# Optimization experiments

Hardware: AMD Instinct MI355X
Metric: run time of the kernel (lower is better)

The kernel has to match this reference:

```python
import jax, jax.numpy as jnp
import numpy as np

K = 1024      # codebook_size
D = 64        # embedding_dim
DECAY = 0.99
EPS = 1e-05


def setup_inputs() -> dict:
    key = jax.random.key(0)
    k1, k2, k3 = jax.random.split(key, 3)
    z_e = jax.random.normal(k1, (16, D, 64, 64), dtype=jnp.float32)
    emb = jax.random.normal(k2, (D, K), dtype=jnp.float32) * 0.05
    emb_ema = emb  # buffer initialized as clone of emb
    counts_ema = jnp.zeros((K,), dtype=jnp.float32)
    return {"z_e": z_e, "emb": emb, "emb_ema": emb_ema, "counts_ema": counts_ema}


def reference(z_e, emb, emb_ema, counts_ema):
    B, Dd, H, W = z_e.shape
    # [B,D,H,W] -> [B*H*W, D]
    z = jnp.transpose(z_e, (0, 2, 3, 1)).reshape(-1, Dd)
    # squared L2 distance to each code: [N, K]
    dist = (z * z).sum(1, keepdims=True) - 2.0 * (z @ emb) + (emb * emb).sum(0, keepdims=True)
    idx = jnp.argmin(dist, axis=1)                      # [N]
    embeddings = emb.T[idx]                             # [N, D]
    z_q = z + jax.lax.stop_gradient(embeddings - z)     # straight-through

    # EMA codebook update (no_grad in original)
    zg = jax.lax.stop_gradient(z)
    counts = jnp.zeros((K,), dtype=emb.dtype).at[idx].add(1.0)          # one-hot column sums
    counts_ema_new = counts_ema + (1.0 - DECAY) * (counts - counts_ema)
    emb_update = jax.ops.segment_sum(zg, idx, num_segments=K).T          # [D, K]
    emb_ema_new = emb_ema + (1.0 - DECAY) * (emb_update - emb_ema)
    n = counts_ema_new.sum()
    counts_norm = (counts_ema_new + EPS) / (n + K * EPS) * n
    emb_new = emb_ema_new / counts_norm[None, :]

    z_q_out = jnp.transpose(z_q.reshape(B, H, W, Dd), (0, 3, 1, 2))      # back to [B,D,H,W]
    idx_out = idx.reshape(B, H, W)
    return z_q_out, idx_out, emb_new, emb_ema_new, counts_ema_new
```

## Files before the change

### kernel.cpp

```cpp
#include <hip/hip_runtime.h>
#include <math.h>

#define KCODES 1024
#define DDIM   64

constexpr size_t O_ZQ  = 0;
constexpr size_t O_IDX = 4194304;
constexpr size_t O_EMB = O_IDX + 65536;
constexpr size_t O_EMA = O_EMB + 65536;
constexpr size_t O_CEN = O_EMA + 65536;

constexpr size_t W_UPD   = 0;
constexpr size_t W_CNT   = 65536;
constexpr size_t W_ENORM = W_CNT + 1024;
constexpr size_t W_EMBT  = W_ENORM + 1024;
constexpr size_t W_E16   = W_EMBT + 65536;
constexpr size_t W_E16L  = W_E16 + 32768;
constexpr size_t W_FLAGN = W_E16L + 32768;
constexpr size_t W_FLAGL = W_FLAGN + 16;
constexpr int    FLAGCAP = 16384;

typedef _Float16 f16;
typedef f16 f16x8 __attribute__((ext_vector_type(8)));
typedef float f32x4 __attribute__((ext_vector_type(4)));

__global__ __launch_bounds__(256) void vq_prep(const float* __restrict__ emb,
                                               float* __restrict__ ws) {
  __shared__ float t_lds[64 * 65];
  const int tid = threadIdx.x;
  const int g   = blockIdx.x;
  const int k0  = g * 64;

  #pragma unroll
  for (int it = 0; it < 16; ++it) {
    const int idx = tid + it * 256;
    const int d   = idx >> 6;
    const int kq  = idx & 63;
    t_lds[d * 65 + kq] = emb[d * KCODES + k0 + kq];
  }
  __syncthreads();

  f16* e16h = (f16*)(ws + W_E16);
  f16* e16l = (f16*)(ws + W_E16L);
  #pragma unroll
  for (int it = 0; it < 16; ++it) {
    const int idx = tid + it * 256;
    const int k   = idx >> 6;
    const int d   = idx & 63;
    const float v = t_lds[d * 65 + k];
    ws[W_EMBT + (size_t)(k0 + k) * 64 + d] = v;
    const f16 hi = (f16)v;
    e16h[(size_t)(k0 + k) * 64 + d] = hi;
    e16l[(size_t)(k0 + k) * 64 + d] = (f16)(v - (float)hi);
  }

  if (tid < 64) {
    const int k = tid;
    float s = 0.f;
    #pragma unroll
    for (int d = 0; d < DDIM; ++d) {
      const float v = t_lds[d * 65 + k];
      s = fmaf(v, v, s);
    }
    ws[W_ENORM + k0 + k] = s;
  }

  float4* u4 = (float4*)(ws + W_UPD);
  #pragma unroll
  for (int j = 0; j < 4; ++j) u4[g * 1024 + tid + j * 256] = float4{0.f, 0.f, 0.f, 0.f};
  if (tid < 64) ws[W_CNT + k0 + tid] = 0.f;
  if (g == 0 && tid == 0) ((int*)(ws + W_FLAGN))[0] = 0;
}

#define ZP 68
__global__ __launch_bounds__(256, 4) void vq_main(
    const float* __restrict__ z_e,
    const float* __restrict__ e16hf,
    const float* __restrict__ e16lf,
    const float* __restrict__ embT,
    const float* __restrict__ eN,
    float* __restrict__ upd,
    float* __restrict__ cnt,
    int*   __restrict__ flagn,
    int*   __restrict__ flagl,
    float* __restrict__ out) {
  __shared__ float z_lds[DDIM * ZP];
  __shared__ __align__(16) f16 e_lds[128 * 64];
  __shared__ __align__(16) f16 el_lds[128 * 64];
  __shared__ __align__(16) float en_lds[128];
  __shared__ int   bidx[64];
  __shared__ float sred[33];

  const int tid  = threadIdx.x;
  const int bid  = blockIdx.x;
  const int wv   = tid >> 6;
  const int lane = tid & 63;
  const int m    = lane & 15;
  const int q    = lane >> 4;
  const int rloc = wv * 16 + m;

  const int n0  = bid * 64;
  const int b   = n0 >> 12;
  const int hw0 = n0 & 4095;
  const size_t zbase = (size_t)b * 262144 + (size_t)hw0;

  {
    const float4* z4 = (const float4*)(z_e + zbase);
    #pragma unroll
    for (int it = 0; it < 4; ++it) {
      const int f  = tid + it * 256;
      const int d  = f >> 4;
      const int r4 = f & 15;
      const float4 v = z4[(size_t)d * 1024 + r4];
      *(float4*)(z_lds + d * ZP + r4 * 4) = v;
    }
  }
  __syncthreads();

  f16x8 bf0h, bf1h, bf0l, bf1l;
  float zz = 0.f;
  #pragma unroll
  for (int j = 0; j < 8; ++j) {
    const float v0 = z_lds[(q * 8 + j) * ZP + rloc];
    const float v1 = z_lds[(32 + q * 8 + j) * ZP + rloc];
    zz = fmaf(v0, v0, zz);
    zz = fmaf(v1, v1, zz);
    const f16 h0 = (f16)v0;
    const f16 h1 = (f16)v1;
    bf0h[j] = h0;
    bf1h[j] = h1;
    bf0l[j] = (f16)(v0 - (float)h0);
    bf1l[j] = (f16)(v1 - (float)h1);
  }
  zz += __shfl_xor(zz, 16, 64);
  zz += __shfl_xor(zz, 32, 64);

  const int lcl7  = m & 7;
  const int aoff0 = m * 128 + ((q)     ^ lcl7) * 16;
  const int aoff1 = m * 128 + ((4 + q) ^ lcl7) * 16;

  float m1 = INFINITY, m2 = INFINITY;
  int   i1 = 0;
  float emax = 0.f;

  const float4* e16g4h = (const float4*)e16hf;
  const float4* e16g4l = (const float4*)e16lf;
  const float4* eNg4   = (const float4*)eN;

  #pragma unroll 1
  for (int c = 0; c < 8; ++c) {
    __syncthreads();
    #pragma unroll
    for (int i = 0; i < 4; ++i) {
      const int u  = i * 256 + tid;
      const int cl = u >> 3;
      const int db = u & 7;
      const int so = cl * 128 + ((db ^ (cl & 7)) * 16);
      const float4 vh = e16g4h[c * 1024 + u];
      const float4 vl = e16g4l[c * 1024 + u];
      *(float4*)((char*)e_lds  + so) = vh;
      *(float4*)((char*)el_lds + so) = vl;
    }
    if (tid < 32) {
      const float4 v = eNg4[c * 32 + tid];
      ((float4*)en_lds)[tid] = v;
      emax = fmaxf(emax, fmaxf(fmaxf(v.x, v.y), fmaxf(v.z, v.w)));
    }
    __syncthreads();

    #pragma unroll
    for (int t = 0; t < 8; ++t) {
      const f16x8 a0h = *(const f16x8*)((const char*)e_lds  + t * 2048 + aoff0);
      const f16x8 a1h = *(const f16x8*)((const char*)e_lds  + t * 2048 + aoff1);
      const f16x8 a0l = *(const f16x8*)((const char*)el_lds + t * 2048 + aoff0);
      const f16x8 a1l = *(const f16x8*)((const char*)el_lds + t * 2048 + aoff1);
      f32x4 acc = {0.f, 0.f, 0.f, 0.f};
      acc = __builtin_amdgcn_mfma_f32_16x16x32_f16(a0l, bf0h, acc, 0, 0, 0);
      acc = __builtin_amdgcn_mfma_f32_16x16x32_f16(a1l, bf1h, acc, 0, 0, 0);
      acc = __builtin_amdgcn_mfma_f32_16x16x32_f16(a0h, bf0l, acc, 0, 0, 0);
      acc = __builtin_amdgcn_mfma_f32_16x16x32_f16(a1h, bf1l, acc, 0, 0, 0);
      acc = __builtin_amdgcn_mfma_f32_16x16x32_f16(a0h, bf0h, acc, 0, 0, 0);
      acc = __builtin_amdgcn_mfma_f32_16x16x32_f16(a1h, bf1h, acc, 0, 0, 0);
      const float4 en4 = *(const float4*)(en_lds + t * 16 + q * 4);
      const float env[4] = {en4.x, en4.y, en4.z, en4.w};
      const int ib = c * 128 + t * 16 + q * 4;
      #pragma unroll
      for (int r = 0; r < 4; ++r) {
        const float v  = fmaf(-2.f, acc[r], env[r]);
        const bool lt  = v < m1;
        m2 = fminf(m2, fmaxf(v, m1));
        if (lt) i1 = ib + r;
        m1 = fminf(m1, v);
      }
    }
  }

  __syncthreads();
  if (tid < 32) sred[tid] = emax;
  __syncthreads();
  if (tid == 0) {
    float mx = sred[0];
    #pragma unroll
    for (int i2 = 1; i2 < 32; ++i2) mx = fmaxf(mx, sred[i2]);
    sred[32] = mx;
  }
  __syncthreads();
  const float emax2 = sred[32];

  #pragma unroll
  for (int off = 16; off <= 32; off <<= 1) {
    const float m1o = __shfl_xor(m1, off, 64);
    const float m2o = __shfl_xor(m2, off, 64);
    const int   i1o = __shfl_xor(i1, off, 64);
    const float nm2 = fminf(fminf(m2, m2o), fmaxf(m1, m1o));
    if (m1o < m1) i1 = i1o;
    m1 = fminf(m1, m1o);
    m2 = nm2;
  }

  if (lane < 16) {
    const int row = rloc;
    const float M = 1.0e-4f * sqrtf(zz) * sqrtf(emax2);
    if (m2 - m1 > M) {
      bidx[row] = i1;
      out[O_IDX + n0 + row] = (float)i1;
      atomicAdd(cnt + i1, 1.0f);
    } else {
      bidx[row] = -1;
      const int s = atomicAdd(flagn, 1);
      if (s < FLAGCAP) flagl[s] = n0 + row;
    }
  }
  __syncthreads();

  {
    const int row  = tid & 63;
    const int dgrp = tid >> 6;
    const int code = bidx[row];
    if (code >= 0) {
      const float4* er4 = (const float4*)(embT + (size_t)code * 64);
      #pragma unroll
      for (int qq = 0; qq < 4; ++qq) {
        const float4 e4 = er4[dgrp * 4 + qq];
        const float ev[4] = {e4.x, e4.y, e4.z, e4.w};
        #pragma unroll
        for (int x = 0; x < 4; ++x) {
          const int d = dgrp * 16 + qq * 4 + x;
          const float zv = z_lds[d * ZP + row];
          out[O_ZQ + zbase + (size_t)d * 4096 + row] = zv + (ev[x] - zv);
        }
      }
    }
  }

  {
    #pragma unroll 4
    for (int rr = 0; rr < 16; ++rr) {
      const int row  = wv * 16 + rr;
      const int code = bidx[row];
      if (code >= 0)
        atomicAdd(upd + (size_t)code * 64 + lane, z_lds[lane * ZP + row]);
    }
  }
}

__global__ __launch_bounds__(256) void vq_rescore(
    const float* __restrict__ z_e,
    const float* __restrict__ embT,
    const float* __restrict__ eN,
    const int* __restrict__ flagn,
    const int* __restrict__ flagl,
    float* __restrict__ upd,
    float* __restrict__ cnt,
    float* __restrict__ out) {
  __shared__ float zrow[64];
  __shared__ float wv_v[4];
  __shared__ int   wv_i[4];
  __shared__ int   bestc;

  const int tid = threadIdx.x;
  int nf = *flagn;
  if (nf > FLAGCAP) nf = FLAGCAP;

  for (int j = blockIdx.x; j < nf; j += gridDim.x) {
    __syncthreads();
    const int rowid = flagl[j];
    const int bb = rowid >> 12;
    const int hw = rowid & 4095;
    const size_t base = (size_t)bb * 262144 + (size_t)hw;
    if (tid < 64) zrow[tid] = z_e[base + (size_t)tid * 4096];
    __syncthreads();

    float bm = INFINITY;
    int   bi = 0;
    #pragma unroll
    for (int cc = 0; cc < 4; ++cc) {
      const int k = tid * 4 + cc;
      const float4* e4p = (const float4*)(embT + (size_t)k * 64);
      float a0 = 0.f, a1 = 0.f, a2 = 0.f, a3 = 0.f;
      #pragma unroll
      for (int d4 = 0; d4 < 16; ++d4) {
        const float4 e4 = e4p[d4];
        a0 = fmaf(zrow[d4 * 4 + 0], e4.x, a0);
        a1 = fmaf(zrow[d4 * 4 + 1], e4.y, a1);
        a2 = fmaf(zrow[d4 * 4 + 2], e4.z, a2);
        a3 = fmaf(zrow[d4 * 4 + 3], e4.w, a3);
      }
      const float dist = fmaf(-2.f, (a0 + a1) + (a2 + a3), eN[k]);
      if (dist < bm) { bm = dist; bi = k; }
    }
    #pragma unroll
    for (int mm = 1; mm < 64; mm <<= 1) {
      const float v2 = __shfl_xor(bm, mm, 64);
      const int   i2 = __shfl_xor(bi, mm, 64);
      if (v2 < bm || (v2 == bm && i2 < bi)) { bm = v2; bi = i2; }
    }
    if ((tid & 63) == 0) { wv_v[tid >> 6] = bm; wv_i[tid >> 6] = bi; }
    __syncthreads();
    if (tid == 0) {
      float v = wv_v[0]; int ix = wv_i[0];
      #pragma unroll
      for (int w = 1; w < 4; ++w) {
        if (wv_v[w] < v || (wv_v[w] == v && wv_i[w] < ix)) { v = wv_v[w]; ix = wv_i[w]; }
      }
      bestc = ix;
      out[O_IDX + rowid] = (float)ix;
      atomicAdd(cnt + ix, 1.0f);
    }
    __syncthreads();
    if (tid < 64) {
      const int d = tid;
      const float zv = zrow[d];
      const float ev = embT[(size_t)bestc * 64 + d];
      out[O_ZQ + base + (size_t)d * 4096] = zv + (ev - zv);
      atomicAdd(upd + (size_t)bestc * 64 + d, zv);
    }
  }
}

__global__ __launch_bounds__(256) void vq_final(const float* __restrict__ emb_ema,
                                                const float* __restrict__ counts_ema,
                                                const float* __restrict__ ws,
                                                float* __restrict__ out) {
  __shared__ float red[256];
  const int tid = threadIdx.x;
  const float* cnt = ws + W_CNT;

  float psum = 0.f;
  for (int t = tid; t < KCODES; t += 256) {
    const float ce  = counts_ema[t];
    const float cen = ce + 0.01f * (cnt[t] - ce);
    psum += cen;
    if (blockIdx.x == 0) out[O_CEN + t] = cen;
  }
  red[tid] = psum;
  __syncthreads();
  #pragma unroll
  for (int s = 128; s > 0; s >>= 1) {
    if (tid < s) red[tid] += red[tid + s];
    __syncthreads();
  }
  const float nsum = red[0];

  const int i = blockIdx.x * 256 + tid;
  const int d = i >> 10;
  const int k = i & 1023;

  const float ce  = counts_ema[k];
  const float cen = ce + 0.01f * (cnt[k] - ce);
  const float norm = (cen + 1e-5f) / (nsum + (float)KCODES * 1e-5f) * nsum;

  const float ema     = emb_ema[i];
  const float ema_new = ema + 0.01f * (ws[W_UPD + (size_t)k * 64 + d] - ema);
  out[O_EMA + i] = ema_new;
  out[O_EMB + i] = ema_new / norm;
}

extern "C" void kernel_launch(void* const* d_in, const int* in_sizes, int n_in,
                              void* d_out, int out_size, void* d_ws, size_t ws_size,
                              hipStream_t stream) {
  const float* z_e        = (const float*)d_in[0];
  const float* emb        = (const float*)d_in[1];
  const float* emb_ema    = (const float*)d_in[2];
  const float* counts_ema = (const float*)d_in[3];
  float* out = (float*)d_out;
  float* ws  = (float*)d_ws;

  vq_prep<<<16, 256, 0, stream>>>(emb, ws);
  vq_main<<<1024, 256, 0, stream>>>(z_e, ws + W_E16, ws + W_E16L,
                                    ws + W_EMBT, ws + W_ENORM,
                                    ws + W_UPD, ws + W_CNT,
                                    (int*)(ws + W_FLAGN), (int*)(ws + W_FLAGL), out);
  vq_rescore<<<1024, 256, 0, stream>>>(z_e, ws + W_EMBT, ws + W_ENORM,
                                       (int*)(ws + W_FLAGN), (int*)(ws + W_FLAGL),
                                       ws + W_UPD, ws + W_CNT, out);
  vq_final<<<256, 256, 0, stream>>>(emb_ema, counts_ema, ws, out);
}
```

Before: 154.7 us.

## Double-buffer codebook via direct LDS loads, 128 rows per block, fuse final into rescore

The main kernel now handles 128 rows per block with two row fragments per wave, which reuses each codebook LDS tile across twice the MFMA work. Codebook tiles are pre-swizzled in prep and streamed with global_load_lds into a double buffer, so loads overlap compute and one barrier per chunk remains. The -0.5*norm term is folded into the accumulator init, and the argmin becomes an argmax over that shifted score. The per-block emax reduction moves into prep. The final EMA kernel is merged into rescore through a last-block-done atomic, which saves one launch but leaves the final 64K-element update to a single block. FLAGCAP is halved and occupancy drops to 2 blocks per CU.

```diff
diff --git a/kernel.cpp b/kernel.cpp
--- a/kernel.cpp
+++ b/kernel.cpp
@@ -12,17 +12,28 @@
 
 constexpr size_t W_UPD   = 0;
 constexpr size_t W_CNT   = 65536;
-constexpr size_t W_ENORM = W_CNT + 1024;
-constexpr size_t W_EMBT  = W_ENORM + 1024;
-constexpr size_t W_E16   = W_EMBT + 65536;
-constexpr size_t W_E16L  = W_E16 + 32768;
-constexpr size_t W_FLAGN = W_E16L + 32768;
-constexpr size_t W_FLAGL = W_FLAGN + 16;
-constexpr int    FLAGCAP = 16384;
+constexpr size_t W_ENORM = 66560;
+constexpr size_t W_EN2   = 67584;
+constexpr size_t W_EMAXA = 68608;
+constexpr size_t W_FLAGN = 68624;
+constexpr size_t W_DONE  = 68640;
+constexpr size_t W_FLAGL = 68656;
+constexpr int    FLAGCAP = 8192;
+constexpr size_t W_EMBT  = 76848;
+constexpr size_t W_G16H  = 142384;
+constexpr size_t W_G16L  = 175152;
 
 typedef _Float16 f16;
 typedef f16 f16x8 __attribute__((ext_vector_type(8)));
 typedef float f32x4 __attribute__((ext_vector_type(4)));
+
+#define MF(a, b, c) __builtin_amdgcn_mfma_f32_16x16x32_f16((a), (b), (c), 0, 0, 0)
+
+static __device__ __forceinline__ void gload16(const void* g, void* l) {
+  __builtin_amdgcn_global_load_lds(
+      (const __attribute__((address_space(1))) void*)g,
+      (__attribute__((address_space(3))) void*)l, 16, 0, 0);
+}
 
 __global__ __launch_bounds__(256) void vq_prep(const float* __restrict__ emb,
                                                float* __restrict__ ws) {
@@ -40,18 +51,21 @@
   }
   __syncthreads();
 
-  f16* e16h = (f16*)(ws + W_E16);
-  f16* e16l = (f16*)(ws + W_E16L);
+  f16* gh = (f16*)(ws + W_G16H);
+  f16* gl = (f16*)(ws + W_G16L);
   #pragma unroll
   for (int it = 0; it < 16; ++it) {
     const int idx = tid + it * 256;
-    const int k   = idx >> 6;
+    const int kk  = idx >> 6;
     const int d   = idx & 63;
-    const float v = t_lds[d * 65 + k];
-    ws[W_EMBT + (size_t)(k0 + k) * 64 + d] = v;
+    const float v = t_lds[d * 65 + kk];
+    ws[W_EMBT + (size_t)(k0 + kk) * 64 + d] = v;
     const f16 hi = (f16)v;
-    e16h[(size_t)(k0 + k) * 64 + d] = hi;
-    e16l[(size_t)(k0 + k) * 64 + d] = (f16)(v - (float)hi);
+    const f16 lo = (f16)(v - (float)hi);
+    const int u  = (d >> 3) ^ (kk & 7);
+    const size_t fo = (size_t)g * 4096 + kk * 64 + u * 8 + (d & 7);
+    gh[fo] = hi;
+    gl[fo] = lo;
   }
 
   if (tid < 64) {
@@ -63,33 +77,41 @@
       s = fmaf(v, v, s);
     }
     ws[W_ENORM + k0 + k] = s;
+    ws[W_EN2   + k0 + k] = -0.5f * s;
+    float mx = s;
+    #pragma unroll
+    for (int off = 1; off < 64; off <<= 1) mx = fmaxf(mx, __shfl_xor(mx, off, 64));
+    if (tid == 0) ws[W_EMAXA + g] = mx;
   }
 
   float4* u4 = (float4*)(ws + W_UPD);
   #pragma unroll
   for (int j = 0; j < 4; ++j) u4[g * 1024 + tid + j * 256] = float4{0.f, 0.f, 0.f, 0.f};
   if (tid < 64) ws[W_CNT + k0 + tid] = 0.f;
-  if (g == 0 && tid == 0) ((int*)(ws + W_FLAGN))[0] = 0;
+  if (g == 0 && tid == 0) {
+    ((int*)(ws + W_FLAGN))[0] = 0;
+    ((int*)(ws + W_DONE))[0]  = 0;
+  }
 }
 
-#define ZP 68
-__global__ __launch_bounds__(256, 4) void vq_main(
+#define ZP 132
+__global__ __launch_bounds__(256, 2) void vq_main(
     const float* __restrict__ z_e,
-    const float* __restrict__ e16hf,
-    const float* __restrict__ e16lf,
+    const float* __restrict__ g16h,
+    const float* __restrict__ g16l,
     const float* __restrict__ embT,
-    const float* __restrict__ eN,
+    const float* __restrict__ en2,
+    const float* __restrict__ emaxa,
     float* __restrict__ upd,
     float* __restrict__ cnt,
     int*   __restrict__ flagn,
     int*   __restrict__ flagl,
     float* __restrict__ out) {
   __shared__ float z_lds[DDIM * ZP];
-  __shared__ __align__(16) f16 e_lds[128 * 64];
-  __shared__ __align__(16) f16 el_lds[128 * 64];
-  __shared__ __align__(16) float en_lds[128];
-  __shared__ int   bidx[64];
-  __shared__ float sred[33];
+  __shared__ __align__(16) f16 e_hi[2][4096];
+  __shared__ __align__(16) f16 e_lo[2][4096];
+  __shared__ __align__(16) float en2_lds[KCODES];
+  __shared__ int bidx[128];
 
   const int tid  = threadIdx.x;
   const int bid  = blockIdx.x;
@@ -97,155 +119,177 @@
   const int lane = tid & 63;
   const int m    = lane & 15;
   const int q    = lane >> 4;
-  const int rloc = wv * 16 + m;
-
-  const int n0  = bid * 64;
+  const int r0   = wv * 32 + m;
+  const int r1   = r0 + 16;
+
+  const int n0  = bid * 128;
   const int b   = n0 >> 12;
   const int hw0 = n0 & 4095;
   const size_t zbase = (size_t)b * 262144 + (size_t)hw0;
 
   {
+    const char* sh = (const char*)g16h + (size_t)(wv * 2) * 1024 + lane * 16;
+    const char* sl = (const char*)g16l + (size_t)(wv * 2) * 1024 + lane * 16;
+    char* dh = (char*)&e_hi[0][0] + (wv * 2) * 1024;
+    char* dl = (char*)&e_lo[0][0] + (wv * 2) * 1024;
+    gload16(sh, dh);           gload16(sh + 1024, dh + 1024);
+    gload16(sl, dl);           gload16(sl + 1024, dl + 1024);
+  }
+
+  {
     const float4* z4 = (const float4*)(z_e + zbase);
     #pragma unroll
-    for (int it = 0; it < 4; ++it) {
+    for (int it = 0; it < 8; ++it) {
       const int f  = tid + it * 256;
-      const int d  = f >> 4;
-      const int r4 = f & 15;
+      const int d  = f >> 5;
+      const int r4 = f & 31;
       const float4 v = z4[(size_t)d * 1024 + r4];
       *(float4*)(z_lds + d * ZP + r4 * 4) = v;
     }
   }
+  ((float4*)en2_lds)[tid] = ((const float4*)en2)[tid];
+
+  float emax = 0.f;
+  {
+    const float4* e4 = (const float4*)emaxa;
+    #pragma unroll
+    for (int i = 0; i < 4; ++i) {
+      const float4 v = e4[i];
+      emax = fmaxf(emax, fmaxf(fmaxf(v.x, v.y), fmaxf(v.z, v.w)));
+    }
+  }
   __syncthreads();
 
-  f16x8 bf0h, bf1h, bf0l, bf1l;
-  float zz = 0.f;
+  f16x8 b0h_0, b1h_0, b0l_0, b1l_0, b0h_1, b1h_1, b0l_1, b1l_1;
+  float zz0 = 0.f, zz1 = 0.f;
   #pragma unroll
   for (int j = 0; j < 8; ++j) {
-    const float v0 = z_lds[(q * 8 + j) * ZP + rloc];
-    const float v1 = z_lds[(32 + q * 8 + j) * ZP + rloc];
-    zz = fmaf(v0, v0, zz);
-    zz = fmaf(v1, v1, zz);
-    const f16 h0 = (f16)v0;
-    const f16 h1 = (f16)v1;
-    bf0h[j] = h0;
-    bf1h[j] = h1;
-    bf0l[j] = (f16)(v0 - (float)h0);
-    bf1l[j] = (f16)(v1 - (float)h1);
-  }
-  zz += __shfl_xor(zz, 16, 64);
-  zz += __shfl_xor(zz, 32, 64);
+    const int d0 = q * 8 + j, d1 = 32 + q * 8 + j;
+    const float v00 = z_lds[d0 * ZP + r0];
+    const float v01 = z_lds[d1 * ZP + r0];
+    const float v10 = z_lds[d0 * ZP + r1];
+    const float v11 = z_lds[d1 * ZP + r1];
+    zz0 = fmaf(v00, v00, zz0); zz0 = fmaf(v01, v01, zz0);
+    zz1 = fmaf(v10, v10, zz1); zz1 = fmaf(v11, v11, zz1);
+    const f16 h00 = (f16)v00, h01 = (f16)v01, h10 = (f16)v10, h11 = (f16)v11;
+    b0h_0[j] = h00; b1h_0[j] = h01; b0h_1[j] = h10; b1h_1[j] = h11;
+    b0l_0[j] = (f16)(v00 - (float)h00);
+    b1l_0[j] = (f16)(v01 - (float)h01);
+    b0l_1[j] = (f16)(v10 - (float)h10);
+    b1l_1[j] = (f16)(v11 - (float)h11);
+  }
+  zz0 += __shfl_xor(zz0, 16, 64); zz0 += __shfl_xor(zz0, 32, 64);
+  zz1 += __shfl_xor(zz1, 16, 64); zz1 += __shfl_xor(zz1, 32, 64);
 
   const int lcl7  = m & 7;
   const int aoff0 = m * 128 + ((q)     ^ lcl7) * 16;
   const int aoff1 = m * 128 + ((4 + q) ^ lcl7) * 16;
 
-  float m1 = INFINITY, m2 = INFINITY;
-  int   i1 = 0;
-  float emax = 0.f;
-
-  const float4* e16g4h = (const float4*)e16hf;
-  const float4* e16g4l = (const float4*)e16lf;
-  const float4* eNg4   = (const float4*)eN;
+  float M1_0 = -INFINITY, M2_0 = -INFINITY, M1_1 = -INFINITY, M2_1 = -INFINITY;
+  int   I1_0 = 0, I1_1 = 0;
 
   #pragma unroll 1
-  for (int c = 0; c < 8; ++c) {
-    __syncthreads();
-    #pragma unroll
-    for (int i = 0; i < 4; ++i) {
-      const int u  = i * 256 + tid;
-      const int cl = u >> 3;
-      const int db = u & 7;
-      const int so = cl * 128 + ((db ^ (cl & 7)) * 16);
-      const float4 vh = e16g4h[c * 1024 + u];
-      const float4 vl = e16g4l[c * 1024 + u];
-      *(float4*)((char*)e_lds  + so) = vh;
-      *(float4*)((char*)el_lds + so) = vl;
-    }
-    if (tid < 32) {
-      const float4 v = eNg4[c * 32 + tid];
-      ((float4*)en_lds)[tid] = v;
-      emax = fmaxf(emax, fmaxf(fmaxf(v.x, v.y), fmaxf(v.z, v.w)));
-    }
-    __syncthreads();
-
-    #pragma unroll
-    for (int t = 0; t < 8; ++t) {
-      const f16x8 a0h = *(const f16x8*)((const char*)e_lds  + t * 2048 + aoff0);
-      const f16x8 a1h = *(const f16x8*)((const char*)e_lds  + t * 2048 + aoff1);
-      const f16x8 a0l = *(const f16x8*)((const char*)el_lds + t * 2048 + aoff0);
-      const f16x8 a1l = *(const f16x8*)((const char*)el_lds + t * 2048 + aoff1);
-      f32x4 acc = {0.f, 0.f, 0.f, 0.f};
-      acc = __builtin_amdgcn_mfma_f32_16x16x32_f16(a0l, bf0h, acc, 0, 0, 0);
-      acc = __builtin_amdgcn_mfma_f32_16x16x32_f16(a1l, bf1h, acc, 0, 0, 0);
-      acc = __builtin_amdgcn_mfma_f32_16x16x32_f16(a0h, bf0l, acc, 0, 0, 0);
-      acc = __builtin_amdgcn_mfma_f32_16x16x32_f16(a1h, bf1l, acc, 0, 0, 0);
-      acc = __builtin_amdgcn_mfma_f32_16x16x32_f16(a0h, bf0h, acc, 0, 0, 0);
-      acc = __builtin_amdgcn_mfma_f32_16x16x32_f16(a1h, bf1h, acc, 0, 0, 0);
-      const float4 en4 = *(const float4*)(en_lds + t * 16 + q * 4);
-      const float env[4] = {en4.x, en4.y, en4.z, en4.w};
-      const int ib = c * 128 + t * 16 + q * 4;
+  for (int c = 0; c < 16; ++c) {
+    const int cb = c & 1;
+    if (c < 15) {
+      const int nb = cb ^ 1;
+      const size_t so = (size_t)(c + 1) * 8192 + (wv * 2) * 1024 + lane * 16;
+      const char* sh = (const char*)g16h + so;
+      const char* sl = (const char*)g16l + so;
+      char* dh = (char*)&e_hi[nb][0] + (wv * 2) * 1024;
+      char* dl = (char*)&e_lo[nb][0] + (wv * 2) * 1024;
+      gload16(sh, dh);           gload16(sh + 1024, dh + 1024);
+      gload16(sl, dl);           gload16(sl + 1024, dl + 1024);
+    }
+    const char* eb = (const char*)&e_hi[cb][0];
+    const char* lb = (const char*)&e_lo[cb][0];
+    #pragma unroll
+    for (int t = 0; t < 4; ++t) {
+      const f16x8 a0h = *(const f16x8*)(eb + t * 2048 + aoff0);
+      const f16x8 a1h = *(const f16x8*)(eb + t * 2048 + aoff1);
+      const f16x8 a0l = *(const f16x8*)(lb + t * 2048 + aoff0);
+      const f16x8 a1l = *(const f16x8*)(lb + t * 2048 + aoff1);
+      const f32x4 en2f = *(const f32x4*)(en2_lds + c * 64 + t * 16 + q * 4);
+      f32x4 acc0 = en2f, acc1 = en2f;
+      acc0 = MF(a0l, b0h_0, acc0);  acc1 = MF(a0l, b0h_1, acc1);
+      acc0 = MF(a1l, b1h_0, acc0);  acc1 = MF(a1l, b1h_1, acc1);
+      acc0 = MF(a0h, b0l_0, acc0);  acc1 = MF(a0h, b0l_1, acc1);
+      acc0 = MF(a1h, b1l_0, acc0);  acc1 = MF(a1h, b1l_1, acc1);
+      acc0 = MF(a0h, b0h_0, acc0);  acc1 = MF(a0h, b0h_1, acc1);
+      acc0 = MF(a1h, b1h_0, acc0);  acc1 = MF(a1h, b1h_1, acc1);
+      const int ib = c * 64 + t * 16 + q * 4;
       #pragma unroll
       for (int r = 0; r < 4; ++r) {
-        const float v  = fmaf(-2.f, acc[r], env[r]);
-        const bool lt  = v < m1;
-        m2 = fminf(m2, fmaxf(v, m1));
-        if (lt) i1 = ib + r;
-        m1 = fminf(m1, v);
+        const float a = acc0[r];
+        const bool gt = a > M1_0;
+        M2_0 = fmaxf(M2_0, fminf(a, M1_0));
+        if (gt) I1_0 = ib + r;
+        M1_0 = fmaxf(M1_0, a);
+        const float a1v = acc1[r];
+        const bool gt1 = a1v > M1_1;
+        M2_1 = fmaxf(M2_1, fminf(a1v, M1_1));
+        if (gt1) I1_1 = ib + r;
+        M1_1 = fmaxf(M1_1, a1v);
       }
     }
-  }
-
-  __syncthreads();
-  if (tid < 32) sred[tid] = emax;
-  __syncthreads();
-  if (tid == 0) {
-    float mx = sred[0];
-    #pragma unroll
-    for (int i2 = 1; i2 < 32; ++i2) mx = fmaxf(mx, sred[i2]);
-    sred[32] = mx;
-  }
-  __syncthreads();
-  const float emax2 = sred[32];
+    __syncthreads();
+  }
 
   #pragma unroll
   for (int off = 16; off <= 32; off <<= 1) {
-    const float m1o = __shfl_xor(m1, off, 64);
-    const float m2o = __shfl_xor(m2, off, 64);
-    const int   i1o = __shfl_xor(i1, off, 64);
-    const float nm2 = fminf(fminf(m2, m2o), fmaxf(m1, m1o));
-    if (m1o < m1) i1 = i1o;
-    m1 = fminf(m1, m1o);
-    m2 = nm2;
-  }
-
-  if (lane < 16) {
-    const int row = rloc;
-    const float M = 1.0e-4f * sqrtf(zz) * sqrtf(emax2);
-    if (m2 - m1 > M) {
-      bidx[row] = i1;
-      out[O_IDX + n0 + row] = (float)i1;
-      atomicAdd(cnt + i1, 1.0f);
+    {
+      const float o1 = __shfl_xor(M1_0, off, 64);
+      const float o2 = __shfl_xor(M2_0, off, 64);
+      const int   oi = __shfl_xor(I1_0, off, 64);
+      const float nm2 = fmaxf(fmaxf(M2_0, o2), fminf(M1_0, o1));
+      if (o1 > M1_0) I1_0 = oi;
+      M1_0 = fmaxf(M1_0, o1);
+      M2_0 = nm2;
+    }
+    {
+      const float o1 = __shfl_xor(M1_1, off, 64);
+      const float o2 = __shfl_xor(M2_1, off, 64);
+      const int   oi = __shfl_xor(I1_1, off, 64);
+      const float nm2 = fmaxf(fmaxf(M2_1, o2), fminf(M1_1, o1));
+      if (o1 > M1_1) I1_1 = oi;
+      M1_1 = fmaxf(M1_1, o1);
+      M2_1 = nm2;
+    }
+  }
+
+  if (lane < 32) {
+    const int s   = lane >> 4;
+    const int row = wv * 32 + s * 16 + m;
+    const float MM1 = s ? M1_1 : M1_0;
+    const float MM2 = s ? M2_1 : M2_0;
+    const int   II  = s ? I1_1 : I1_0;
+    const float zzv = s ? zz1 : zz0;
+    const float Mh = 5.0e-5f * sqrtf(zzv * emax);
+    if (MM1 - MM2 > Mh) {
+      bidx[row] = II;
+      out[O_IDX + n0 + row] = (float)II;
+      atomicAdd(cnt + II, 1.0f);
     } else {
       bidx[row] = -1;
-      const int s = atomicAdd(flagn, 1);
-      if (s < FLAGCAP) flagl[s] = n0 + row;
+      const int sl = atomicAdd(flagn, 1);
+      if (sl < FLAGCAP) flagl[sl] = n0 + row;
     }
   }
   __syncthreads();
 
   {
-    const int row  = tid & 63;
-    const int dgrp = tid >> 6;
+    const int row  = tid & 127;
+    const int half = tid >> 7;
     const int code = bidx[row];
     if (code >= 0) {
       const float4* er4 = (const float4*)(embT + (size_t)code * 64);
       #pragma unroll
-      for (int qq = 0; qq < 4; ++qq) {
-        const float4 e4 = er4[dgrp * 4 + qq];
+      for (int qq = 0; qq < 8; ++qq) {
+        const float4 e4 = er4[half * 8 + qq];
         const float ev[4] = {e4.x, e4.y, e4.z, e4.w};
         #pragma unroll
         for (int x = 0; x < 4; ++x) {
-          const int d = dgrp * 16 + qq * 4 + x;
+          const int d = half * 32 + qq * 4 + x;
           const float zv = z_lds[d * ZP + row];
           out[O_ZQ + zbase + (size_t)d * 4096 + row] = zv + (ev[x] - zv);
         }
@@ -255,8 +299,8 @@
 
   {
     #pragma unroll 4
-    for (int rr = 0; rr < 16; ++rr) {
-      const int row  = wv * 16 + rr;
+    for (int rr = 0; rr < 32; ++rr) {
+      const int row  = wv * 32 + rr;
       const int code = bidx[row];
       if (code >= 0)
         atomicAdd(upd + (size_t)code * 64 + lane, z_lds[lane * ZP + row]);
@@ -264,7 +308,7 @@
   }
 }
 
-__global__ __launch_bounds__(256) void vq_rescore(
+__global__ __launch_bounds__(256) void vq_rescore_final(
     const float* __restrict__ z_e,
     const float* __restrict__ embT,
     const float* __restrict__ eN,
@@ -272,11 +316,16 @@
     const int* __restrict__ flagl,
     float* __restrict__ upd,
     float* __restrict__ cnt,
+    const float* __restrict__ emb_ema,
+    const float* __restrict__ counts_ema,
+    int* __restrict__ done,
     float* __restrict__ out) {
   __shared__ float zrow[64];
   __shared__ float wv_v[4];
   __shared__ int   wv_i[4];
   __shared__ int   bestc;
+  __shared__ int   lastf;
+  __shared__ float red[256];
 
   const int tid = threadIdx.x;
   int nf = *flagn;
@@ -336,44 +385,43 @@
       atomicAdd(upd + (size_t)bestc * 64 + d, zv);
     }
   }
-}
-
-__global__ __launch_bounds__(256) void vq_final(const float* __restrict__ emb_ema,
-                                                const float* __restrict__ counts_ema,
-                                                const float* __restrict__ ws,
-                                                float* __restrict__ out) {
-  __shared__ float red[256];
-  const int tid = threadIdx.x;
-  const float* cnt = ws + W_CNT;
-
-  float psum = 0.f;
-  for (int t = tid; t < KCODES; t += 256) {
-    const float ce  = counts_ema[t];
-    const float cen = ce + 0.01f * (cnt[t] - ce);
-    psum += cen;
-    if (blockIdx.x == 0) out[O_CEN + t] = cen;
-  }
-  red[tid] = psum;
+
   __syncthreads();
-  #pragma unroll
-  for (int s = 128; s > 0; s >>= 1) {
-    if (tid < s) red[tid] += red[tid + s];
-    __syncthreads();
-  }
-  const float nsum = red[0];
-
-  const int i = blockIdx.x * 256 + tid;
-  const int d = i >> 10;
-  const int k = i & 1023;
-
-  const float ce  = counts_ema[k];
-  const float cen = ce + 0.01f * (cnt[k] - ce);
-  const float norm = (cen + 1e-5f) / (nsum + (float)KCODES * 1e-5f) * nsum;
-
-  const float ema     = emb_ema[i];
-  const float ema_new = ema + 0.01f * (ws[W_UPD + (size_t)k * 64 + d] - ema);
-  out[O_EMA + i] = ema_new;
-  out[O_EMB + i] = ema_new / norm;
+  __threadfence();
+  if (tid == 0) {
+    const int my = atomicAdd(done, 1);
+    lastf = (my == (int)gridDim.x - 1) ? 1 : 0;
+  }
+  __syncthreads();
+  if (lastf) {
+    __threadfence();
+    float psum = 0.f;
+    for (int t = tid; t < KCODES; t += 256) {
+      const float ce  = counts_ema[t];
+      const float cen = ce + 0.01f * (cnt[t] - ce);
+      psum += cen;
+      out[O_CEN + t] = cen;
+    }
+    red[tid] = psum;
+    __syncthreads();
+    #pragma unroll
+    for (int s = 128; s > 0; s >>= 1) {
+      if (tid < s) red[tid] += red[tid + s];
+      __syncthreads();
+    }
+    const float nsum = red[0];
+    for (int i = tid; i < 65536; i += 256) {
+      const int d = i >> 10;
+      const int k = i & 1023;
+      const float ce  = counts_ema[k];
+      const float cen = ce + 0.01f * (cnt[k] - ce);
+      const float norm = (cen + 1e-5f) / (nsum + (float)KCODES * 1e-5f) * nsum;
+      const float ema     = emb_ema[i];
+      const float ema_new = ema + 0.01f * (upd[(size_t)k * 64 + d] - ema);
+      out[O_EMA + i] = ema_new;
+      out[O_EMB + i] = ema_new / norm;
+    }
+  }
 }
 
 extern "C" void kernel_launch(void* const* d_in, const int* in_sizes, int n_in,
@@ -387,12 +435,13 @@
   float* ws  = (float*)d_ws;
 
   vq_prep<<<16, 256, 0, stream>>>(emb, ws);
-  vq_main<<<1024, 256, 0, stream>>>(z_e, ws + W_E16, ws + W_E16L,
-                                    ws + W_EMBT, ws + W_ENORM,
-                                    ws + W_UPD, ws + W_CNT,
-                                    (int*)(ws + W_FLAGN), (int*)(ws + W_FLAGL), out);
-  vq_rescore<<<1024, 256, 0, stream>>>(z_e, ws + W_EMBT, ws + W_ENORM,
-                                       (int*)(ws + W_FLAGN), (int*)(ws + W_FLAGL),
-                                       ws + W_UPD, ws + W_CNT, out);
-  vq_final<<<256, 256, 0, stream>>>(emb_ema, counts_ema, ws, out);
+  vq_main<<<512, 256, 0, stream>>>(z_e, ws + W_G16H, ws + W_G16L,
+                                   ws + W_EMBT, ws + W_EN2, ws + W_EMAXA,
+                                   ws + W_UPD, ws + W_CNT,
+                                   (int*)(ws + W_FLAGN), (int*)(ws + W_FLAGL), out);
+  vq_rescore_final<<<256, 256, 0, stream>>>(z_e, ws + W_EMBT, ws + W_ENORM,
+                                            (int*)(ws + W_FLAGN), (int*)(ws + W_FLAGL),
+                                            ws + W_UPD, ws + W_CNT,
+                                            emb_ema, counts_ema,
+                                            (int*)(ws + W_DONE), out);
 }
```

New measurement: 253.0 us. 1.64x slower.
